# Performance work log

Hardware: AMD Instinct MI355X
Metric: run time of the kernel (lower is better)

## Reference

```python
import jax, jax.numpy as jnp
import numpy as np

B, T, N, D = 32, 12, 325, 64
H = 4           # geo_num_heads == t_num_heads
HD = D // H     # head_dim = 16
M_SP = 32       # spatial frequency modes (min(32, N//2))
M_T = T // 2    # temporal frequency modes (all low modes)
SCALE = HD ** -0.5


def _lin(x, W):
    # torch nn.Linear (no bias): y = x @ W.T, W: [out, in]
    return jnp.einsum('btnd,ed->btne', x, W)


def _spatial(x, Wq, Wk, Wv, weights_Q, sp_modes):
    # FEDformer-style frequency attention over the node axis N
    q, k, v = _lin(x, Wq), _lin(x, Wk), _lin(x, Wv)          # [B,T,N,D]
    prep = lambda y: y.reshape(B, T, N, H, HD).transpose(0, 1, 3, 4, 2)  # [B,T,H,HD,N]
    qn = prep(q) / jnp.linalg.norm(q)   # global Frobenius norm (torch.norm with no dim)
    kn = prep(k) / jnp.linalg.norm(k)
    vn = prep(v)
    # rfft over nodes, gather selected modes (scatter-into-zeros in torch == gather here
    # since target indices are 0..M-1)
    qf = jnp.fft.rfft(qn, axis=-1)[..., sp_modes]            # [B,T,H,HD,M] c64
    kf = jnp.fft.rfft(kn, axis=-1)[..., sp_modes]
    vf = jnp.fft.rfft(vn, axis=-1)[..., sp_modes]
    M = M_SP
    qg = qf.transpose(0, 1, 2, 4, 3)[:, :, :, :, None, :]    # [B,T,H,M,1,HD]
    wq = jnp.broadcast_to(weights_Q.astype(jnp.complex64), (B, T, H, M, M - 1, HD))
    q_cat = jnp.concatenate([qg, wq], axis=4)                # [B,T,H,M,M,HD]
    kg = kf.transpose(0, 1, 2, 4, 3)[:, :, :, None, :, :]    # [B,T,H,1,M,HD]
    att = kg * jnp.conj(q_cat) * SCALE                       # [B,T,H,M,M,HD] c64
    att = jax.nn.softmax(jnp.abs(att), axis=-2).astype(jnp.complex64)
    att = att.transpose(0, 1, 2, 3, 5, 4)                    # [B,T,H,M,HD,M]
    vg = vf[:, :, :, None, :, :]                             # [B,T,H,1,HD,M]
    out = (vg * jnp.conj(att)).mean(axis=3)                  # [B,T,H,HD,M]
    out_ft = jnp.zeros((B, T, H, HD, N // 2 + 1), jnp.complex64).at[..., sp_modes].set(out)
    y = jnp.fft.irfft(out_ft, n=N, axis=-1)                  # [B,T,H,HD,N]
    return y.transpose(0, 1, 4, 2, 3).reshape(B, T, N, D)


def _temporal(x, Wq, Wk, Wv, weights_Q_t, t_modes):
    # frequency attention over the time axis T with causal (tril) mask.
    # NOTE: torch reshapes the [B,T,N,D] buffer directly as [B,N,T,H,HD] (raw view),
    # so we replicate that exact buffer reinterpretation.
    q, k, v = _lin(x, Wq), _lin(x, Wk), _lin(x, Wv)
    prep = lambda y: y.reshape(B, N, T, H, HD).transpose(0, 1, 3, 4, 2)  # [B,N,H,HD,T]
    qn = prep(q); kn = prep(k); vn = prep(v)
    qn = qn / jnp.linalg.norm(qn)
    kn = kn / jnp.linalg.norm(kn)
    qf = jnp.fft.rfft(qn, axis=-1)[..., t_modes]             # [B,N,H,HD,Mt]
    kf = jnp.fft.rfft(kn, axis=-1)[..., t_modes]
    vf = jnp.fft.rfft(vn, axis=-1)[..., t_modes]
    Mt = M_T
    qg = qf.transpose(0, 1, 2, 4, 3)[:, :, :, :, None, :]    # [B,N,H,Mt,1,HD]
    wq = jnp.broadcast_to(weights_Q_t.astype(jnp.complex64), (B, N, H, Mt, Mt - 1, HD))
    q_cat = jnp.concatenate([qg, wq], axis=4)                # [B,N,H,Mt,Mt,HD]
    kg = kf.transpose(0, 1, 2, 4, 3)[:, :, :, :, None, :]    # [B,N,H,Mt,1,HD] (unsqueeze(4) in torch)
    att = kg * jnp.conj(q_cat) * SCALE                       # [B,N,H,Mt,Mt,HD]
    att = att.transpose(0, 1, 2, 5, 3, 4)                    # [B,N,H,HD,Mt,Mt]
    mask = jnp.tril(jnp.ones((Mt, Mt), jnp.float32))
    att = att * mask                                         # zero above diagonal
    attw = jax.nn.softmax(jnp.abs(att), axis=-1).astype(jnp.complex64)
    vg = vf[..., None]                                       # [B,N,H,HD,Mt,1]
    out = (vg * jnp.conj(attw)).mean(axis=-1)                # [B,N,H,HD,Mt]
    out_ft = jnp.zeros((B, N, H, HD, T // 2 + 1), jnp.complex64).at[..., t_modes].set(out)
    y = jnp.fft.irfft(out_ft, n=T, axis=-1)                  # [B,N,H,HD,T]
    return y.transpose(0, 4, 1, 2, 3).reshape(B, T, N, D)


def _gcn(x, adj, W_fc1, W_mlp, b_mlp):
    a = adj / jnp.sum(adj, axis=1, keepdims=True)            # row-normalized
    agg = jnp.einsum('btkd,nk->btnd', x, a)
    h = jnp.einsum('btnd,ed->btne', agg, W_fc1)              # fc1 (no bias)
    return jnp.einsum('btnd,ed->btne', h, W_mlp) + b_mlp     # mlp (bias)


def _forward(x, adj, Wq_geo, Wk_geo, Wv_geo, Wq_t, Wk_t, Wv_t,
             W_fc1, W_mlp, b_mlp, weights_Q, weights_Q_t, sp_modes, t_modes):
    gcn_out = _gcn(x, adj, W_fc1, W_mlp, b_mlp)
    sp_x = _spatial(x, Wq_geo, Wk_geo, Wv_geo, weights_Q, sp_modes)
    te_x = _temporal(x, Wq_t, Wk_t, Wv_t, weights_Q_t, t_modes)
    return gcn_out + sp_x + te_x   # proj_drop is identity (p=0)


def setup_inputs() -> dict:
    key = jax.random.key(0)
    ks = jax.random.split(key, 13)
    w = lambda k, s: jax.random.normal(k, s, dtype=jnp.float32) * 0.05
    rng = np.random.default_rng(0)
    sp_modes = np.sort(rng.permutation(N // 2)[:M_SP]).astype(np.int32)
    t_modes = np.arange(M_T, dtype=np.int32)  # modes_T == T//2 selects all low modes
    return {
        'x': jax.random.normal(ks[0], (B, T, N, D), dtype=jnp.float32),
        'adj': jax.random.uniform(ks[1], (N, N), dtype=jnp.float32),
        'Wq_geo': w(ks[2], (D, D)), 'Wk_geo': w(ks[3], (D, D)), 'Wv_geo': w(ks[4], (D, D)),
        'Wq_t': w(ks[5], (D, D)), 'Wk_t': w(ks[6], (D, D)), 'Wv_t': w(ks[7], (D, D)),
        'W_fc1': w(ks[8], (D, D)), 'W_mlp': w(ks[9], (D, D)), 'b_mlp': w(ks[10], (D,)),
        'weights_Q': jax.random.normal(ks[11], (M_SP, M_SP - 1, HD), dtype=jnp.float32),
        'weights_Q_t': jax.random.normal(ks[12], (M_T, M_T - 1, HD), dtype=jnp.float32),
        'sp_modes': jnp.asarray(sp_modes),
        't_modes': jnp.asarray(t_modes),
    }


def reference(x, adj, Wq_geo, Wk_geo, Wv_geo, Wq_t, Wk_t, Wv_t,
              W_fc1, W_mlp, b_mlp, weights_Q, weights_Q_t, sp_modes, t_modes):
    return _forward(x, adj, Wq_geo, Wk_geo, Wv_geo, Wq_t, Wk_t, Wv_t,
                    W_fc1, W_mlp, b_mlp, weights_Q, weights_Q_t, sp_modes, t_modes)
```

## Files before the change

kernel.cpp:

```cpp
#include <hip/hip_runtime.h>


typedef unsigned short u16;
typedef short short8 __attribute__((ext_vector_type(8)));
typedef float floatx4 __attribute__((ext_vector_type(4)));

__device__ __forceinline__ u16 f2bf(float f) {
  union { float fp; unsigned int u; } v; v.fp = f;
  unsigned int x = v.u;
  x += 0x7FFF + ((x >> 16) & 1);
  return (u16)(x >> 16);
}

constexpr size_t OFF_NORM = 4096;
constexpr size_t OFF_WC   = 4112;
constexpr size_t OFF_WQA  = 8208;
constexpr size_t OFF_ANB  = 24080;
constexpr size_t OFF_TB   = 81280;
constexpr size_t OFF_T2   = 102080;
constexpr size_t OFF_OFT  = 112480;
constexpr size_t OFF_XCT  = 898912;
constexpr size_t OFF_VT   = 5224288;
constexpr size_t OFF_ALT  = 13211488;

__global__ __launch_bounds__(256) void k_prep(const float* __restrict__ adj,
                                              const float* __restrict__ Wmlp,
                                              const float* __restrict__ Wfc1,
                                              const float* __restrict__ wQ,
                                              const int* __restrict__ sp_modes,
                                              float* __restrict__ ws) {
  __shared__ float red[256];
  const int tid = threadIdx.x;
  const int blk = blockIdx.x;
  if (blk == 0) {
    for (int o = tid; o < 4096; o += 256) {
      int g = o >> 6, dd = o & 63;
      float s = 0.f;
      for (int e = 0; e < 64; ++e)
        s = fmaf(Wmlp[g * 64 + e], Wfc1[e * 64 + dd], s);
      ws[OFF_WC + o] = s;
    }
  } else if (blk < 9) {
    for (int i = (blk - 1) * 256 + tid; i < 15872; i += 2048)
      ws[OFF_WQA + i] = fabsf(wQ[i]);
  } else if (blk < 334) {
    const int n = blk - 9;
    float p = 0.f;
    for (int k = tid; k < 325; k += 256) p += adj[n * 325 + k];
    red[tid] = p;
    __syncthreads();
    for (int s2 = 128; s2 > 0; s2 >>= 1) {
      if (tid < s2) red[tid] += red[tid + s2];
      __syncthreads();
    }
    const float inv = 1.f / red[0];
    u16* ANB = (u16*)(ws + OFF_ANB);
    for (int k = tid; k < 352; k += 256)
      ANB[(size_t)n * 352 + k] = (k < 325) ? f2bf(adj[n * 325 + k] * inv) : (u16)0;
  } else {
    const int j = blk - 334;
    const int f = sp_modes[j];
    const float wgt = (f == 0) ? 1.f : 2.f;
    u16* T2B = (u16*)(ws + OFF_T2);
    u16* TB = (u16*)(ws + OFF_TB);
    const int row_re = 8 * (j >> 2) + (j & 3);
    const int row_im = row_re + 4;
    for (int n = tid; n < 352; n += 256) {
      float c = 0.f, s = 0.f;
      if (n < 325) {
        int mm = (f * n) % 325;
        float th = 6.283185307179586f * (float)mm * (1.f / 325.f);
        c = cosf(th);
        s = sinf(th);
      }
      TB[(size_t)row_re * 352 + n] = f2bf(c);
      TB[(size_t)row_im * 352 + n] = f2bf(-s);
      if (n < 325) {
        T2B[(size_t)n * 64 + 2 * j] = f2bf(wgt * (1.f / 325.f) * c);
        T2B[(size_t)n * 64 + 2 * j + 1] = f2bf(-wgt * (1.f / 325.f) * s);
      }
    }
  }
}

__global__ __launch_bounds__(256) void k_linear2(const float* __restrict__ x,
                                                 const float* __restrict__ Wvt,
                                                 const float* __restrict__ Wq,
                                                 const float* __restrict__ Wk,
                                                 float* __restrict__ ws) {
  __shared__ __align__(16) u16 XA[128 * 72];
  __shared__ __align__(16) u16 WB[256 * 72];
  __shared__ float reds[8];
  const int tid = threadIdx.x;
  const int wv = tid >> 6, lane = tid & 63, lc = lane & 15, quad = lane >> 4;
  const size_t base = (size_t)blockIdx.x * 128;

  for (int i = tid; i < 2048; i += 256) {
    const int row = i >> 4, e0 = (i & 15) * 4;
    const float4 v = *(const float4*)(x + (base + row) * 64 + e0);
    u16* dst = &XA[row * 72 + e0];
    dst[0] = f2bf(v.x); dst[1] = f2bf(v.y); dst[2] = f2bf(v.z); dst[3] = f2bf(v.w);
  }
  for (int i = tid; i < 4096; i += 256) {
    const int row = i >> 4, e0 = (i & 15) * 4;
    const int g = row & 63, sel = row >> 6;
    const float* src = (sel == 0) ? (ws + OFF_WC + g * 64)
                     : (sel == 1) ? (Wvt + g * 64)
                     : (sel == 2) ? (Wq + g * 64)
                                  : (Wk + g * 64);
    const float4 v = *(const float4*)(src + e0);
    u16* dst = &WB[row * 72 + e0];
    dst[0] = f2bf(v.x); dst[1] = f2bf(v.y); dst[2] = f2bf(v.z); dst[3] = f2bf(v.w);
  }
  __syncthreads();

  floatx4 acc[2][16] = {};
#pragma unroll
  for (int kc = 0; kc < 2; ++kc) {
    short8 af[2];
#pragma unroll
    for (int mi = 0; mi < 2; ++mi)
      af[mi] = *(const short8*)&XA[(32 * wv + 16 * mi + lc) * 72 + kc * 32 + quad * 8];
#pragma unroll
    for (int ni = 0; ni < 16; ++ni) {
      const short8 bf_ = *(const short8*)&WB[(ni * 16 + lc) * 72 + kc * 32 + quad * 8];
#pragma unroll
      for (int mi = 0; mi < 2; ++mi)
        acc[mi][ni] = __builtin_amdgcn_mfma_f32_16x16x32_bf16(af[mi], bf_, acc[mi][ni], 0, 0, 0);
    }
  }

  float sq = 0.f, sk = 0.f;
#pragma unroll
  for (int mi = 0; mi < 2; ++mi)
#pragma unroll
    for (int reg = 0; reg < 4; ++reg) {
      const int row = 32 * wv + 16 * mi + quad * 4 + reg;
#pragma unroll
      for (int ni = 0; ni < 4; ++ni)
        ws[OFF_VT + (base + row) * 64 + ni * 16 + lc] = acc[mi][4 + ni][reg];
#pragma unroll
      for (int ni = 0; ni < 4; ++ni) {
        const float v = acc[mi][8 + ni][reg];
        sq = fmaf(v, v, sq);
      }
#pragma unroll
      for (int ni = 0; ni < 4; ++ni) {
        const float v = acc[mi][12 + ni][reg];
        sk = fmaf(v, v, sk);
      }
    }
  for (int off = 32; off > 0; off >>= 1) {
    sq += __shfl_down(sq, off);
    sk += __shfl_down(sk, off);
  }
  if (lane == 0) { reds[wv] = sq; reds[4 + wv] = sk; }
  __syncthreads();
  if (tid == 0) atomicAdd(&ws[OFF_NORM + 0], reds[0] + reds[1] + reds[2] + reds[3]);
  if (tid == 1) atomicAdd(&ws[OFF_NORM + 1], reds[4] + reds[5] + reds[6] + reds[7]);

  u16* xcT = WB;
#pragma unroll
  for (int mi = 0; mi < 2; ++mi)
#pragma unroll
    for (int ni = 0; ni < 4; ++ni)
#pragma unroll
      for (int reg = 0; reg < 4; ++reg)
        xcT[(ni * 16 + lc) * 132 + 32 * wv + 16 * mi + quad * 4 + reg] =
            f2bf(acc[mi][ni][reg]);
  __syncthreads();
  u16* XCT = (u16*)(ws + OFF_XCT);
  for (int i = tid; i < 8192; i += 256) {
    const int d = i >> 7, r = i & 127;
    const unsigned int row = (unsigned int)(base + r);
    const unsigned int bt = row / 325u;
    const unsigned int n = row - bt * 325u;
    XCT[(size_t)bt * 22528 + (size_t)d * 352 + n] = xcT[d * 132 + r];
  }
}

__global__ __launch_bounds__(256) void k_spatial3(const float* __restrict__ x,
                                                  const float* __restrict__ Wq,
                                                  const float* __restrict__ Wk,
                                                  const float* __restrict__ Wv,
                                                  float* __restrict__ ws) {
  __shared__ __align__(16) float smem[10240];
  const int tid = threadIdx.x;
  const int bt = blockIdx.x;
  const int lane = tid & 63, wv = tid >> 6;
  const int lc = lane & 15, quad = lane >> 4;

  u16* Atile = (u16*)smem;
  u16* Btile = (u16*)smem + 2560;
  const u16* TB = (const u16*)(ws + OFF_TB);
  const float* xb = x + (size_t)bt * 20800;
  floatx4 accA[4] = {};
  {
    const int arow = tid >> 2, ac8 = (tid & 3) * 8;
    const int br = tid & 31, be0 = (tid >> 5) * 8;
    for (int kc = 0; kc < 11; ++kc) {
      const int k0 = kc * 32;
      __syncthreads();
      *(uint4*)&Atile[arow * 40 + ac8] = *(const uint4*)&TB[(size_t)arow * 352 + k0 + ac8];
      {
        float v[8];
        if (k0 + br < 325) {
          const float* src = xb + (size_t)(k0 + br) * 64 + be0;
          *(float4*)v = *(const float4*)src;
          *(float4*)(v + 4) = *(const float4*)(src + 4);
        } else {
#pragma unroll
          for (int u = 0; u < 8; ++u) v[u] = 0.f;
        }
#pragma unroll
        for (int u = 0; u < 8; ++u) Btile[(be0 + u) * 40 + br] = f2bf(v[u]);
      }
      __syncthreads();
      const short8 af = *(const short8*)&Atile[(16 * wv + lc) * 40 + quad * 8];
#pragma unroll
      for (int t = 0; t < 4; ++t) {
        const short8 bf_ = *(const short8*)&Btile[(t * 16 + lc) * 40 + quad * 8];
        accA[t] = __builtin_amdgcn_mfma_f32_16x16x32_bf16(af, bf_, accA[t], 0, 0, 0);
      }
    }
  }
  __syncthreads();
  u16* xfl2 = (u16*)smem;
  u16* Wt3b = (u16*)smem + 5120;
#pragma unroll
  for (int t = 0; t < 4; ++t)
#pragma unroll
    for (int r = 0; r < 4; ++r)
      xfl2[(t >> 1) * 2560 + (16 * wv + quad * 4 + r) * 40 + (t & 1) * 16 + lc] =
          f2bf(accA[t][r]);
  for (int i = tid; i < 3072; i += 256) {
    const int row = i >> 4, e0 = (i & 15) * 4;
    const float* Wm = (row < 64) ? Wq : (row < 128) ? Wk : Wv;
    const float4 v = *(const float4*)(Wm + (size_t)(row & 63) * 64 + e0);
    u16* dst = &Wt3b[(e0 >> 5) * 7680 + row * 40 + (e0 & 31)];
    dst[0] = f2bf(v.x); dst[1] = f2bf(v.y); dst[2] = f2bf(v.z); dst[3] = f2bf(v.w);
  }
  __syncthreads();

  floatx4 acc2[12] = {};
#pragma unroll
  for (int kc2 = 0; kc2 < 2; ++kc2) {
    const short8 af2 = *(const short8*)&xfl2[kc2 * 2560 + (16 * wv + lc) * 40 + quad * 8];
#pragma unroll
    for (int t = 0; t < 12; ++t) {
      const short8 bf2 = *(const short8*)&Wt3b[kc2 * 7680 + (t * 16 + lc) * 40 + quad * 8];
      acc2[t] = __builtin_amdgcn_mfma_f32_16x16x32_bf16(af2, bf2, acc2[t], 0, 0, 0);
    }
  }
  __syncthreads();

  float* sq_q = smem;
  float* sq_k = smem + 2048;
  float* vfre = smem + 4096;
  float* vfim = smem + 6144;
  float* wbar = smem + 8192;
  for (int i = tid; i < 2048; i += 256) wbar[i] = 0.f;
  {
    const int fb = 8 * wv + ((quad >= 2) ? 4 : 0);
    const int isim = quad & 1;
#pragma unroll
    for (int t = 0; t < 12; ++t) {
      const int mat = t >> 2;
      const int d = (t & 3) * 16 + lc;
#pragma unroll
      for (int r = 0; r < 4; ++r) {
        const float v = acc2[t][r];
        if (mat == 2) {
          if (isim) vfim[(fb + r) * 64 + d] = v;
          else vfre[(fb + r) * 64 + d] = v;
        } else {
          const float s2 = v * v + __shfl_xor(v * v, 16);
          if (!isim) {
            if (mat == 0) sq_q[(fb + r) * 64 + d] = s2;
            else sq_k[(fb + r) * 64 + d] = s2;
          }
        }
      }
    }
  }
  __syncthreads();
  const float inv_nq = rsqrtf(ws[OFF_NORM + 0]);
  const float inv_nk = rsqrtf(ws[OFF_NORM + 1]);
  for (int i = tid; i < 2048; i += 256)
    sq_k[i] = 0.25f * inv_nk * sqrtf(sq_k[i]);
  __syncthreads();
  {
    const int d = tid & 63, fb2 = tid >> 6, hd = d & 15;
    const float* wqa = ws + OFF_WQA;
    float wacc[32];
#pragma unroll
    for (int j = 0; j < 32; ++j) wacc[j] = 0.f;
    for (int r8 = 0; r8 < 8; ++r8) {
      const int m = fb2 + (r8 << 2);
      const float aq = inv_nq * sqrtf(sq_q[m * 64 + d]);
      float sv[32];
      float mx = -1e30f;
#pragma unroll
      for (int j = 0; j < 32; ++j) {
        const float a = (j == 0) ? aq : wqa[(m * 31 + (j - 1)) * 16 + hd];
        const float s = sq_k[j * 64 + d] * a;
        sv[j] = s;
        mx = fmaxf(mx, s);
      }
      float sum = 0.f;
#pragma unroll
      for (int j = 0; j < 32; ++j) {
        const float ev = __expf(sv[j] - mx);
        sv[j] = ev;
        sum += ev;
      }
      const float sc = 0.03125f / sum;
#pragma unroll
      for (int j = 0; j < 32; ++j) wacc[j] += sv[j] * sc;
    }
#pragma unroll
    for (int j = 0; j < 32; ++j) atomicAdd(&wbar[j * 64 + d], wacc[j]);
  }
  __syncthreads();
  unsigned int* OFTu = (unsigned int*)(ws + OFF_OFT) + (size_t)bt * 2048;
  for (int i2 = tid; i2 < 2048; i2 += 256) {
    const int d = i2 >> 5, j = i2 & 31;
    const float w = wbar[j * 64 + d];
    const unsigned int lo = f2bf(vfre[j * 64 + d] * w);
    const unsigned int hi = f2bf(vfim[j * 64 + d] * w);
    OFTu[i2] = lo | (hi << 16);
  }
}

__global__ __launch_bounds__(256) void k_alt(float* __restrict__ ws) {
  const int idx = blockIdx.x * 256 + threadIdx.x;
  if (idx >= 32 * 325 * 64) return;
  const int dd = idx & 63;
  const int n = (idx >> 6) % 325;
  const int b = idx / (64 * 325);
  const float* vt = ws + OFF_VT + ((size_t)b * 3900 + (size_t)n * 12) * 64 + dd;
  float s = 0.f, sign = 1.f;
  for (int k = 0; k < 12; ++k) {
    s += sign * vt[k * 64];
    sign = -sign;
  }
  ws[OFF_ALT + idx] = s;
}

__global__ __launch_bounds__(256) void k_final2(const float* __restrict__ bmlp,
                                                float* __restrict__ ws,
                                                float* __restrict__ out) {
  __shared__ __align__(16) u16 Atile[128 * 32];
  __shared__ __align__(16) u16 Btile[64 * 32];
  const int tid = threadIdx.x;
  const int bt = blockIdx.x / 3, mc = blockIdx.x % 3;
  const int m0 = mc * 128;
  const int wave = tid >> 6, lane = tid & 63;
  const int quad = lane >> 4, lc = lane & 15;

  const u16* ANB = (const u16*)(ws + OFF_ANB);
  const u16* T2B = (const u16*)(ws + OFF_T2);
  const u16* XCT = (const u16*)(ws + OFF_XCT) + (size_t)bt * 22528;
  const u16* OFT = (const u16*)(ws + OFF_OFT) + (size_t)bt * 4096;

  floatx4 acc[2][4] = {};

  for (int c13 = 0; c13 < 13; ++c13) {
    const bool gcn = (c13 < 11);
    const u16* Asrc = gcn ? ANB : T2B;
    const int astr = gcn ? 352 : 64;
    const int acol = gcn ? c13 * 32 : (c13 - 11) * 32;
    const u16* Bsrc = gcn ? XCT : OFT;
    const int bstr = gcn ? 352 : 64;
    __syncthreads();
    for (int i = tid; i < 512; i += 256) {
      const int row = i >> 2, c8 = (i & 3) * 8;
      const int gr = m0 + row;
      uint4 v = make_uint4(0, 0, 0, 0);
      if (gr < 325)
        v = *(const uint4*)(Asrc + (size_t)gr * astr + acol + c8);
      *(uint4*)&Atile[row * 32 + c8] = v;
    }
    {
      const int d = tid >> 2, c8 = (tid & 3) * 8;
      *(uint4*)&Btile[d * 32 + c8] =
          *(const uint4*)(Bsrc + (size_t)d * bstr + acol + c8);
    }
    __syncthreads();
    short8 af[2], bf_[4];
#pragma unroll
    for (int mi = 0; mi < 2; ++mi)
      af[mi] = *(const short8*)&Atile[(wave * 32 + mi * 16 + lc) * 32 + quad * 8];
#pragma unroll
    for (int ni = 0; ni < 4; ++ni)
      bf_[ni] = *(const short8*)&Btile[(ni * 16 + lc) * 32 + quad * 8];
#pragma unroll
    for (int mi = 0; mi < 2; ++mi)
#pragma unroll
      for (int ni = 0; ni < 4; ++ni)
        acc[mi][ni] = __builtin_amdgcn_mfma_f32_16x16x32_bf16(
            af[mi], bf_[ni], acc[mi][ni], 0, 0, 0);
  }

  const int b = bt / 12, t = bt - b * 12;
  const float sgn = (t & 1) ? -1.f : 1.f;
#pragma unroll
  for (int ni = 0; ni < 4; ++ni) {
    const int d = ni * 16 + lc;
    const float bias = bmlp[d];
#pragma unroll
    for (int mi = 0; mi < 2; ++mi) {
#pragma unroll
      for (int reg = 0; reg < 4; ++reg) {
        const int n = m0 + wave * 32 + mi * 16 + quad * 4 + reg;
        if (n >= 325) continue;
        const float v = ws[OFF_VT + ((size_t)b * 3900 + (size_t)n * 12 + t) * 64 + d];
        const float al = ws[OFF_ALT + ((size_t)b * 325 + n) * 64 + d];
        const float te = (v - sgn * al * (1.f / 12.f)) * (1.f / 6.f);
        out[((size_t)bt * 325 + n) * 64 + d] = acc[mi][ni][reg] + bias + te;
      }
    }
  }
}

extern "C" void kernel_launch(void* const* d_in, const int* in_sizes, int n_in,
                              void* d_out, int out_size, void* d_ws, size_t ws_size,
                              hipStream_t stream) {
  const float* x = (const float*)d_in[0];
  const float* adj = (const float*)d_in[1];
  const float* Wq_g = (const float*)d_in[2];
  const float* Wk_g = (const float*)d_in[3];
  const float* Wv_g = (const float*)d_in[4];
  const float* Wv_t = (const float*)d_in[7];
  const float* Wfc1 = (const float*)d_in[8];
  const float* Wmlp = (const float*)d_in[9];
  const float* bmlp = (const float*)d_in[10];
  const float* wQ = (const float*)d_in[11];
  const int* sp_modes = (const int*)d_in[13];
  float* ws = (float*)d_ws;
  float* out = (float*)d_out;

  (void)in_sizes; (void)n_in; (void)out_size; (void)ws_size;

  hipMemsetAsync(ws + OFF_NORM, 0, 2 * sizeof(float), stream);
  hipMemsetAsync(ws + OFF_XCT, 0, (size_t)384 * 22528 * sizeof(u16), stream);
  k_prep<<<366, 256, 0, stream>>>(adj, Wmlp, Wfc1, wQ, sp_modes, ws);
  k_linear2<<<975, 256, 0, stream>>>(x, Wv_t, Wq_g, Wk_g, ws);
  k_spatial3<<<384, 256, 0, stream>>>(x, Wq_g, Wk_g, Wv_g, ws);
  k_alt<<<2600, 256, 0, stream>>>(ws);
  k_final2<<<1152, 256, 0, stream>>>(bmlp, ws, out);
}
```

Baseline: 272.2 us.

## Precompute bf16 weights once, drop XCT memset, and stream operands from global

```diff
diff --git a/kernel.cpp b/kernel.cpp
--- a/kernel.cpp
+++ b/kernel.cpp
@@ -13,7 +13,6 @@
 }
 
 constexpr size_t OFF_NORM = 4096;
-constexpr size_t OFF_WC   = 4112;
 constexpr size_t OFF_WQA  = 8208;
 constexpr size_t OFF_ANB  = 24080;
 constexpr size_t OFF_TB   = 81280;
@@ -22,23 +21,30 @@
 constexpr size_t OFF_XCT  = 898912;
 constexpr size_t OFF_VT   = 5224288;
 constexpr size_t OFF_ALT  = 13211488;
+constexpr size_t OFF_WBB  = OFF_ALT;
+constexpr size_t OFF_WSPB = OFF_ALT + 8192;
 
 __global__ __launch_bounds__(256) void k_prep(const float* __restrict__ adj,
                                               const float* __restrict__ Wmlp,
                                               const float* __restrict__ Wfc1,
                                               const float* __restrict__ wQ,
+                                              const float* __restrict__ Wvt,
+                                              const float* __restrict__ Wq,
+                                              const float* __restrict__ Wk,
+                                              const float* __restrict__ Wv,
                                               const int* __restrict__ sp_modes,
                                               float* __restrict__ ws) {
   __shared__ float red[256];
   const int tid = threadIdx.x;
   const int blk = blockIdx.x;
+  u16* WBBu = (u16*)(ws + OFF_WBB);
   if (blk == 0) {
     for (int o = tid; o < 4096; o += 256) {
       int g = o >> 6, dd = o & 63;
       float s = 0.f;
       for (int e = 0; e < 64; ++e)
         s = fmaf(Wmlp[g * 64 + e], Wfc1[e * 64 + dd], s);
-      ws[OFF_WC + o] = s;
+      WBBu[o] = f2bf(s);
     }
   } else if (blk < 9) {
     for (int i = (blk - 1) * 256 + tid; i < 15872; i += 2048)
@@ -57,7 +63,7 @@
     u16* ANB = (u16*)(ws + OFF_ANB);
     for (int k = tid; k < 352; k += 256)
       ANB[(size_t)n * 352 + k] = (k < 325) ? f2bf(adj[n * 325 + k] * inv) : (u16)0;
-  } else {
+  } else if (blk < 366) {
     const int j = blk - 334;
     const int f = sp_modes[j];
     const float wgt = (f == 0) ? 1.f : 2.f;
@@ -80,97 +86,94 @@
         T2B[(size_t)n * 64 + 2 * j + 1] = f2bf(-wgt * (1.f / 325.f) * s);
       }
     }
-  }
-}
-
-__global__ __launch_bounds__(256) void k_linear2(const float* __restrict__ x,
-                                                 const float* __restrict__ Wvt,
-                                                 const float* __restrict__ Wq,
-                                                 const float* __restrict__ Wk,
-                                                 float* __restrict__ ws) {
+  } else if (blk == 366) {
+    for (int i = tid; i < 12288; i += 256) {
+      const int r = i >> 6, e = i & 63;
+      const float* src = (r < 64) ? Wvt : (r < 128) ? Wq : Wk;
+      WBBu[4096 + i] = f2bf(src[(size_t)(r & 63) * 64 + e]);
+    }
+  } else if (blk == 367) {
+    u16* WSPBu = (u16*)(ws + OFF_WSPB);
+    for (int i = tid; i < 12288; i += 256) {
+      const int r = i >> 6, e = i & 63;
+      const float* src = (r < 64) ? Wq : (r < 128) ? Wk : Wv;
+      WSPBu[i] = f2bf(src[(size_t)(r & 63) * 64 + e]);
+    }
+  } else {
+    const int idx = (blk - 368) * 256 + tid;
+    u16* p = (u16*)(ws + OFF_XCT) + (size_t)(idx >> 6) * 22528 + (size_t)(idx & 63) * 352;
+    for (int c = 325; c < 352; ++c) p[c] = 0;
+  }
+}
+
+__global__ __launch_bounds__(512, 3) void k_linear2(const float* __restrict__ x,
+                                                    float* __restrict__ ws) {
   __shared__ __align__(16) u16 XA[128 * 72];
-  __shared__ __align__(16) u16 WB[256 * 72];
-  __shared__ float reds[8];
+  __shared__ float reds[16];
   const int tid = threadIdx.x;
   const int wv = tid >> 6, lane = tid & 63, lc = lane & 15, quad = lane >> 4;
   const size_t base = (size_t)blockIdx.x * 128;
-
-  for (int i = tid; i < 2048; i += 256) {
+  const u16* WBBu = (const u16*)(ws + OFF_WBB);
+
+  for (int i = tid; i < 2048; i += 512) {
     const int row = i >> 4, e0 = (i & 15) * 4;
     const float4 v = *(const float4*)(x + (base + row) * 64 + e0);
     u16* dst = &XA[row * 72 + e0];
     dst[0] = f2bf(v.x); dst[1] = f2bf(v.y); dst[2] = f2bf(v.z); dst[3] = f2bf(v.w);
   }
-  for (int i = tid; i < 4096; i += 256) {
-    const int row = i >> 4, e0 = (i & 15) * 4;
-    const int g = row & 63, sel = row >> 6;
-    const float* src = (sel == 0) ? (ws + OFF_WC + g * 64)
-                     : (sel == 1) ? (Wvt + g * 64)
-                     : (sel == 2) ? (Wq + g * 64)
-                                  : (Wk + g * 64);
-    const float4 v = *(const float4*)(src + e0);
-    u16* dst = &WB[row * 72 + e0];
-    dst[0] = f2bf(v.x); dst[1] = f2bf(v.y); dst[2] = f2bf(v.z); dst[3] = f2bf(v.w);
-  }
-  __syncthreads();
-
-  floatx4 acc[2][16] = {};
+  __syncthreads();
+
+  floatx4 acc[16] = {};
 #pragma unroll
   for (int kc = 0; kc < 2; ++kc) {
-    short8 af[2];
-#pragma unroll
-    for (int mi = 0; mi < 2; ++mi)
-      af[mi] = *(const short8*)&XA[(32 * wv + 16 * mi + lc) * 72 + kc * 32 + quad * 8];
+    const short8 af = *(const short8*)&XA[(16 * wv + lc) * 72 + kc * 32 + quad * 8];
 #pragma unroll
     for (int ni = 0; ni < 16; ++ni) {
-      const short8 bf_ = *(const short8*)&WB[(ni * 16 + lc) * 72 + kc * 32 + quad * 8];
-#pragma unroll
-      for (int mi = 0; mi < 2; ++mi)
-        acc[mi][ni] = __builtin_amdgcn_mfma_f32_16x16x32_bf16(af[mi], bf_, acc[mi][ni], 0, 0, 0);
+      const short8 bf_ = *(const short8*)&WBBu[(ni * 16 + lc) * 64 + kc * 32 + quad * 8];
+      acc[ni] = __builtin_amdgcn_mfma_f32_16x16x32_bf16(af, bf_, acc[ni], 0, 0, 0);
     }
   }
 
   float sq = 0.f, sk = 0.f;
 #pragma unroll
-  for (int mi = 0; mi < 2; ++mi)
-#pragma unroll
-    for (int reg = 0; reg < 4; ++reg) {
-      const int row = 32 * wv + 16 * mi + quad * 4 + reg;
-#pragma unroll
-      for (int ni = 0; ni < 4; ++ni)
-        ws[OFF_VT + (base + row) * 64 + ni * 16 + lc] = acc[mi][4 + ni][reg];
-#pragma unroll
-      for (int ni = 0; ni < 4; ++ni) {
-        const float v = acc[mi][8 + ni][reg];
-        sq = fmaf(v, v, sq);
-      }
-#pragma unroll
-      for (int ni = 0; ni < 4; ++ni) {
-        const float v = acc[mi][12 + ni][reg];
-        sk = fmaf(v, v, sk);
-      }
-    }
+  for (int reg = 0; reg < 4; ++reg) {
+    const int row = 16 * wv + quad * 4 + reg;
+#pragma unroll
+    for (int ni = 0; ni < 4; ++ni)
+      ws[OFF_VT + (base + row) * 64 + ni * 16 + lc] = acc[4 + ni][reg];
+#pragma unroll
+    for (int ni = 0; ni < 4; ++ni) {
+      const float v = acc[8 + ni][reg];
+      sq = fmaf(v, v, sq);
+    }
+#pragma unroll
+    for (int ni = 0; ni < 4; ++ni) {
+      const float v = acc[12 + ni][reg];
+      sk = fmaf(v, v, sk);
+    }
+  }
   for (int off = 32; off > 0; off >>= 1) {
     sq += __shfl_down(sq, off);
     sk += __shfl_down(sk, off);
   }
-  if (lane == 0) { reds[wv] = sq; reds[4 + wv] = sk; }
-  __syncthreads();
-  if (tid == 0) atomicAdd(&ws[OFF_NORM + 0], reds[0] + reds[1] + reds[2] + reds[3]);
-  if (tid == 1) atomicAdd(&ws[OFF_NORM + 1], reds[4] + reds[5] + reds[6] + reds[7]);
-
-  u16* xcT = WB;
-#pragma unroll
-  for (int mi = 0; mi < 2; ++mi)
-#pragma unroll
-    for (int ni = 0; ni < 4; ++ni)
-#pragma unroll
-      for (int reg = 0; reg < 4; ++reg)
-        xcT[(ni * 16 + lc) * 132 + 32 * wv + 16 * mi + quad * 4 + reg] =
-            f2bf(acc[mi][ni][reg]);
+  if (lane == 0) { reds[wv] = sq; reds[8 + wv] = sk; }
+  __syncthreads();
+  if (tid == 0)
+    atomicAdd(&ws[OFF_NORM + 0], reds[0] + reds[1] + reds[2] + reds[3] +
+                                 reds[4] + reds[5] + reds[6] + reds[7]);
+  if (tid == 1)
+    atomicAdd(&ws[OFF_NORM + 1], reds[8] + reds[9] + reds[10] + reds[11] +
+                                 reds[12] + reds[13] + reds[14] + reds[15]);
+
+  u16* xcT = XA;
+#pragma unroll
+  for (int ni = 0; ni < 4; ++ni)
+#pragma unroll
+    for (int reg = 0; reg < 4; ++reg)
+      xcT[(ni * 16 + lc) * 132 + 16 * wv + quad * 4 + reg] = f2bf(acc[ni][reg]);
   __syncthreads();
   u16* XCT = (u16*)(ws + OFF_XCT);
-  for (int i = tid; i < 8192; i += 256) {
+  for (int i = tid; i < 8192; i += 512) {
     const int d = i >> 7, r = i & 127;
     const unsigned int row = (unsigned int)(base + r);
     const unsigned int bt = row / 325u;
@@ -180,9 +183,6 @@
 }
 
 __global__ __launch_bounds__(256) void k_spatial3(const float* __restrict__ x,
-                                                  const float* __restrict__ Wq,
-                                                  const float* __restrict__ Wk,
-                                                  const float* __restrict__ Wv,
                                                   float* __restrict__ ws) {
   __shared__ __align__(16) float smem[10240];
   const int tid = threadIdx.x;
@@ -190,56 +190,49 @@
   const int lane = tid & 63, wv = tid >> 6;
   const int lc = lane & 15, quad = lane >> 4;
 
-  u16* Atile = (u16*)smem;
-  u16* Btile = (u16*)smem + 2560;
+  u16* Bt = (u16*)smem;
+  u16* xfl2 = (u16*)smem + 5120;
   const u16* TB = (const u16*)(ws + OFF_TB);
+  const u16* WSPBu = (const u16*)(ws + OFF_WSPB);
   const float* xb = x + (size_t)bt * 20800;
+  const int br = tid & 31, be0 = (tid >> 5) * 8;
+
+  auto stageB = [&](int kc, u16* dst) {
+    const int k0 = kc * 32;
+    float v[8];
+    if (k0 + br < 325) {
+      const float* src = xb + (size_t)(k0 + br) * 64 + be0;
+      *(float4*)v = *(const float4*)src;
+      *(float4*)(v + 4) = *(const float4*)(src + 4);
+    } else {
+#pragma unroll
+      for (int u = 0; u < 8; ++u) v[u] = 0.f;
+    }
+#pragma unroll
+    for (int u = 0; u < 8; ++u) dst[(be0 + u) * 40 + br] = f2bf(v[u]);
+  };
+
   floatx4 accA[4] = {};
-  {
-    const int arow = tid >> 2, ac8 = (tid & 3) * 8;
-    const int br = tid & 31, be0 = (tid >> 5) * 8;
-    for (int kc = 0; kc < 11; ++kc) {
-      const int k0 = kc * 32;
-      __syncthreads();
-      *(uint4*)&Atile[arow * 40 + ac8] = *(const uint4*)&TB[(size_t)arow * 352 + k0 + ac8];
-      {
-        float v[8];
-        if (k0 + br < 325) {
-          const float* src = xb + (size_t)(k0 + br) * 64 + be0;
-          *(float4*)v = *(const float4*)src;
-          *(float4*)(v + 4) = *(const float4*)(src + 4);
-        } else {
-#pragma unroll
-          for (int u = 0; u < 8; ++u) v[u] = 0.f;
-        }
-#pragma unroll
-        for (int u = 0; u < 8; ++u) Btile[(be0 + u) * 40 + br] = f2bf(v[u]);
-      }
-      __syncthreads();
-      const short8 af = *(const short8*)&Atile[(16 * wv + lc) * 40 + quad * 8];
-#pragma unroll
-      for (int t = 0; t < 4; ++t) {
-        const short8 bf_ = *(const short8*)&Btile[(t * 16 + lc) * 40 + quad * 8];
-        accA[t] = __builtin_amdgcn_mfma_f32_16x16x32_bf16(af, bf_, accA[t], 0, 0, 0);
-      }
-    }
-  }
-  __syncthreads();
-  u16* xfl2 = (u16*)smem;
-  u16* Wt3b = (u16*)smem + 5120;
+  stageB(0, Bt);
+  __syncthreads();
+  for (int kc = 0; kc < 11; ++kc) {
+    u16* cur = Bt + (kc & 1) * 2560;
+    if (kc < 10) stageB(kc + 1, Bt + ((kc + 1) & 1) * 2560);
+    const short8 af = *(const short8*)&TB[(size_t)(16 * wv + lc) * 352 + kc * 32 + quad * 8];
+#pragma unroll
+    for (int t = 0; t < 4; ++t) {
+      const short8 bf_ = *(const short8*)&cur[(t * 16 + lc) * 40 + quad * 8];
+      accA[t] = __builtin_amdgcn_mfma_f32_16x16x32_bf16(af, bf_, accA[t], 0, 0, 0);
+    }
+    __syncthreads();
+  }
+
 #pragma unroll
   for (int t = 0; t < 4; ++t)
 #pragma unroll
     for (int r = 0; r < 4; ++r)
       xfl2[(t >> 1) * 2560 + (16 * wv + quad * 4 + r) * 40 + (t & 1) * 16 + lc] =
           f2bf(accA[t][r]);
-  for (int i = tid; i < 3072; i += 256) {
-    const int row = i >> 4, e0 = (i & 15) * 4;
-    const float* Wm = (row < 64) ? Wq : (row < 128) ? Wk : Wv;
-    const float4 v = *(const float4*)(Wm + (size_t)(row & 63) * 64 + e0);
-    u16* dst = &Wt3b[(e0 >> 5) * 7680 + row * 40 + (e0 & 31)];
-    dst[0] = f2bf(v.x); dst[1] = f2bf(v.y); dst[2] = f2bf(v.z); dst[3] = f2bf(v.w);
-  }
   __syncthreads();
 
   floatx4 acc2[12] = {};
@@ -248,7 +241,7 @@
     const short8 af2 = *(const short8*)&xfl2[kc2 * 2560 + (16 * wv + lc) * 40 + quad * 8];
 #pragma unroll
     for (int t = 0; t < 12; ++t) {
-      const short8 bf2 = *(const short8*)&Wt3b[kc2 * 7680 + (t * 16 + lc) * 40 + quad * 8];
+      const short8 bf2 = *(const short8*)&WSPBu[(t * 16 + lc) * 64 + kc2 * 32 + quad * 8];
       acc2[t] = __builtin_amdgcn_mfma_f32_16x16x32_bf16(af2, bf2, acc2[t], 0, 0, 0);
     }
   }
@@ -350,8 +343,6 @@
 __global__ __launch_bounds__(256) void k_final2(const float* __restrict__ bmlp,
                                                 float* __restrict__ ws,
                                                 float* __restrict__ out) {
-  __shared__ __align__(16) u16 Atile[128 * 32];
-  __shared__ __align__(16) u16 Btile[64 * 32];
   const int tid = threadIdx.x;
   const int bt = blockIdx.x / 3, mc = blockIdx.x % 3;
   const int m0 = mc * 128;
@@ -365,6 +356,7 @@
 
   floatx4 acc[2][4] = {};
 
+#pragma unroll
   for (int c13 = 0; c13 < 13; ++c13) {
     const bool gcn = (c13 < 11);
     const u16* Asrc = gcn ? ANB : T2B;
@@ -372,28 +364,18 @@
     const int acol = gcn ? c13 * 32 : (c13 - 11) * 32;
     const u16* Bsrc = gcn ? XCT : OFT;
     const int bstr = gcn ? 352 : 64;
-    __syncthreads();
-    for (int i = tid; i < 512; i += 256) {
-      const int row = i >> 2, c8 = (i & 3) * 8;
-      const int gr = m0 + row;
-      uint4 v = make_uint4(0, 0, 0, 0);
+    short8 af[2], bf_[4];
+#pragma unroll
+    for (int mi = 0; mi < 2; ++mi) {
+      const int gr = m0 + wave * 32 + mi * 16 + lc;
+      short8 a = {};
       if (gr < 325)
-        v = *(const uint4*)(Asrc + (size_t)gr * astr + acol + c8);
-      *(uint4*)&Atile[row * 32 + c8] = v;
-    }
-    {
-      const int d = tid >> 2, c8 = (tid & 3) * 8;
-      *(uint4*)&Btile[d * 32 + c8] =
-          *(const uint4*)(Bsrc + (size_t)d * bstr + acol + c8);
-    }
-    __syncthreads();
-    short8 af[2], bf_[4];
-#pragma unroll
-    for (int mi = 0; mi < 2; ++mi)
-      af[mi] = *(const short8*)&Atile[(wave * 32 + mi * 16 + lc) * 32 + quad * 8];
+        a = *(const short8*)&Asrc[(size_t)gr * astr + acol + quad * 8];
+      af[mi] = a;
+    }
 #pragma unroll
     for (int ni = 0; ni < 4; ++ni)
-      bf_[ni] = *(const short8*)&Btile[(ni * 16 + lc) * 32 + quad * 8];
+      bf_[ni] = *(const short8*)&Bsrc[(size_t)(ni * 16 + lc) * bstr + acol + quad * 8];
 #pragma unroll
     for (int mi = 0; mi < 2; ++mi)
 #pragma unroll
@@ -443,10 +425,10 @@
   (void)in_sizes; (void)n_in; (void)out_size; (void)ws_size;
 
   hipMemsetAsync(ws + OFF_NORM, 0, 2 * sizeof(float), stream);
-  hipMemsetAsync(ws + OFF_XCT, 0, (size_t)384 * 22528 * sizeof(u16), stream);
-  k_prep<<<366, 256, 0, stream>>>(adj, Wmlp, Wfc1, wQ, sp_modes, ws);
-  k_linear2<<<975, 256, 0, stream>>>(x, Wv_t, Wq_g, Wk_g, ws);
-  k_spatial3<<<384, 256, 0, stream>>>(x, Wq_g, Wk_g, Wv_g, ws);
+  k_prep<<<464, 256, 0, stream>>>(adj, Wmlp, Wfc1, wQ, Wv_t, Wq_g, Wk_g, Wv_g,
+                                  sp_modes, ws);
+  k_linear2<<<975, 512, 0, stream>>>(x, ws);
+  k_spatial3<<<384, 256, 0, stream>>>(x, ws);
   k_alt<<<2600, 256, 0, stream>>>(ws);
   k_final2<<<1152, 256, 0, stream>>>(bmlp, ws, out);
 }
```

After: 278.5 us. 1.02x slower.
